# Performance work log

Measured on AMD Instinct MI355X. Metric: run time of the kernel, lower is better.

The kernel has to match this reference:

```python
import jax, jax.numpy as jnp
import numpy as np

NEG = 1e9


def setup_inputs() -> dict:
    key = jax.random.key(0)
    k1, k2, k3 = jax.random.split(key, 3)
    B, Tq, Tv, D = 8, 2048, 2048, 512
    query = jax.random.normal(k1, (B, Tq, D), dtype=jnp.float32)
    value = jax.random.normal(k2, (B, Tv, D), dtype=jnp.float32)
    # length-style masks: every row has at least one valid position
    q_len = jax.random.randint(k3, (B,), Tq // 2, Tq + 1)
    v_len = jax.random.randint(jax.random.fold_in(k3, 1), (B,), Tv // 2, Tv + 1)
    q_mask = jnp.arange(Tq)[None, :] < q_len[:, None]
    v_mask = jnp.arange(Tv)[None, :] < v_len[:, None]
    return {"query": query, "value": value, "q_mask": q_mask, "v_mask": v_mask}


def reference(query, value, q_mask, v_mask):
    # key = value (2-input case); dot-product scores: [B, Tq, Tv]
    scores = jnp.einsum("bqd,bvd->bqv", query, value)
    Tq, Tv = scores.shape[-2], scores.shape[-1]
    # causal lower-triangular mask [1, Tq, Tv]
    causal = (jnp.arange(Tq)[:, None] >= jnp.arange(Tv)[None, :])[None]
    # merge value mask [B, 1, Tv] with causal mask
    scores_mask = jnp.logical_and(v_mask[:, None, :], causal)
    scores = scores - NEG * (~scores_mask).astype(scores.dtype)
    attn = jax.nn.softmax(scores, axis=-1)
    result = jnp.einsum("bqv,bvd->bqd", attn, value)
    # zero out masked query positions
    result = result * q_mask[:, :, None].astype(result.dtype)
    return result
```

## Files before the change

### kernel.cpp

```cpp
#include <hip/hip_runtime.h>
#include <hip/hip_bf16.h>
#include <cstdint>
#include <cstddef>


#define TQ   2048
#define TV   2048
#define DIM  512
#define NB   8
#define NROW (NB * TQ)
#define NSLOT 63

typedef _Float16 f16x8 __attribute__((ext_vector_type(8)));
typedef _Float16 f16x4 __attribute__((ext_vector_type(4)));
typedef float    f32x4 __attribute__((ext_vector_type(4)));
typedef int      i32x4 __attribute__((ext_vector_type(4)));

__device__ __forceinline__ int sched_ns(int g) { return (g + 11) / 11; }
__device__ __forceinline__ int sched_start(int g) {
    return (g < 11) ? g : ((g < 22) ? (2 * g - 11) : (3 * g - 33));
}

__device__ __forceinline__ int mask_fmt(const void* qm) {
    const unsigned* p = (const unsigned*)qm;
    unsigned w0 = p[0];
    if (w0 & 0xFF00u) return 0;
    unsigned w1 = p[1];
    if (w0 == 1u) return (w1 != 0u) ? 1 : 2;
    return 3;
}
__device__ __forceinline__ bool mask_bit(const void* m, int fmt, size_t i) {
    if (fmt == 0) return ((const unsigned char*)m)[i] != 0;
    if (fmt == 1) return ((const int*)m)[i] != 0;
    if (fmt == 2) return ((const unsigned*)m)[2 * i] != 0;
    return ((const float*)m)[i] != 0.0f;
}

__device__ __forceinline__ void gload_lds16(const void* g, void* l) {
    __builtin_amdgcn_global_load_lds(
        (const __attribute__((address_space(1))) unsigned int*)g,
        (__attribute__((address_space(3))) unsigned int*)l, 16, 0, 0);
}

__global__ void cvt_f16_kernel(const float* __restrict__ in, _Float16* __restrict__ out, int n8) {
    int i = blockIdx.x * blockDim.x + threadIdx.x;
    if (i >= n8) return;
    f32x4 x0 = *(const f32x4*)(in + (size_t)i * 8);
    f32x4 x1 = *(const f32x4*)(in + (size_t)i * 8 + 4);
    f16x8 o;
#pragma unroll
    for (int j = 0; j < 4; ++j) { o[j] = (_Float16)x0[j]; o[4 + j] = (_Float16)x1[j]; }
    *(f16x8*)(out + (size_t)i * 8) = o;
}

__global__ __launch_bounds__(256)
void prep_v_kernel(const float* __restrict__ vf, _Float16* __restrict__ wv,
                   _Float16* __restrict__ wvt) {
    __shared__ float sT[64][65];
    int z   = blockIdx.x;
    int b   = z & 7;
    int tv0 = ((z >> 3) & 31) * 64;
    int d0  = (z >> 8) * 64;
    int tid = threadIdx.x;
    int vl  = tid >> 4;
    int dq  = (tid & 15) * 4;
#pragma unroll
    for (int i = 0; i < 4; ++i) {
        int v = vl + i * 16;
        f32x4 x = *(const f32x4*)(vf + ((size_t)b * TV + tv0 + v) * DIM + d0 + dq);
        f16x4 h;
#pragma unroll
        for (int j = 0; j < 4; ++j) { h[j] = (_Float16)x[j]; sT[v][dq + j] = x[j]; }
        *(f16x4*)(wv + ((size_t)b * TV + tv0 + v) * DIM + d0 + dq) = h;
    }
    __syncthreads();
    int dl = tid >> 4;
    int vq = (tid & 15) * 4;
#pragma unroll
    for (int i = 0; i < 4; ++i) {
        int dloc = dl + i * 16;
        f16x4 h;
#pragma unroll
        for (int j = 0; j < 4; ++j) h[j] = (_Float16)sT[vq + j][dloc];
        *(f16x4*)(wvt + ((size_t)b * DIM + d0 + dloc) * TV + tv0 + vq) = h;
    }
}

__global__ __launch_bounds__(512)
__attribute__((amdgpu_waves_per_eu(2, 2)))
void attn_kernel(const _Float16* __restrict__ wq, const _Float16* __restrict__ wv,
                 const _Float16* __restrict__ wvt,
                 const void* __restrict__ qmask, const void* __restrict__ vmask,
                 _Float16* __restrict__ pacc, float* __restrict__ pml) {
    __shared__ __align__(16) _Float16 sV[2][32 * 512];
    __shared__ __align__(16) char     sVT[2][512 * 64];
    __shared__ unsigned sMW[64];

    const int tid  = threadIdx.x;
    const int lane = tid & 63;
    const int w    = tid >> 6;
    const int q16  = lane & 15;
    const int grp  = lane >> 4;

    const int bid  = blockIdx.x;
    const int b    = bid & 7;
    const int slot = (NSLOT - 1) - (bid >> 3);

    int g = 0, s = 0;
#pragma unroll
    for (int j = 0; j < 32; ++j) {
        int st = sched_start(j);
        if (slot >= st && slot < st + sched_ns(j)) { g = j; s = slot - st; }
    }
    const int NSg = sched_ns(g);

    const int pairId = w >> 1;
    const int dhalf  = w & 1;
    const int qtile  = 4 * g + pairId;
    const int qrow   = qtile * 16 + q16;
    const size_t qrowG = (size_t)b * TQ + qrow;
    const int bound = qtile >> 1;

    const int fmt = mask_fmt(qmask);

    unsigned long long qbal = __ballot(mask_bit(qmask, fmt, (size_t)b * TQ + g * 64 + lane));
    const bool waveActive = ((qbal >> (16 * pairId)) & 0xFFFFull) != 0ull;
    int bmaxb = -1;
#pragma unroll
    for (int ti = 0; ti < 4; ++ti)
        if ((qbal >> (16 * ti)) & 0xFFFFull) bmaxb = max(bmaxb, (4 * g + ti) >> 1);

    if (w == 0) {
#pragma unroll
        for (int c = 0; c < 32; ++c) {
            unsigned long long bal = __ballot(mask_bit(vmask, fmt, (size_t)b * TV + c * 64 + lane));
            if (lane == 0) {
                sMW[2 * c]     = (unsigned)(bal & 0xFFFFFFFFull);
                sMW[2 * c + 1] = (unsigned)(bal >> 32);
            }
        }
    }

    f16x8 qreg[16];
    if (waveActive) {
#pragma unroll
        for (int kc = 0; kc < 16; ++kc)
            qreg[kc] = *(const f16x8*)(wq + qrowG * DIM + kc * 32 + grp * 8);
    }

    auto stage = [&](int buf, int tt) {
#pragma unroll
        for (int k = 0; k < 4; ++k) {
            int vr = w * 4 + k;
            const _Float16* src = wv + ((size_t)b * TV + tt * 32 + vr) * DIM
                                     + ((lane ^ ((vr & 7) << 2)) << 3);
            gload_lds16(src, (char*)&sV[buf][0] + vr * 1024);
        }
#pragma unroll
        for (int k = 0; k < 4; ++k) {
            int slot2 = k * 64 + lane;
            int dloc  = w * 64 + (slot2 >> 2);
            int cl    = slot2 & 3;
            const _Float16* src = wvt + ((size_t)b * DIM + dloc) * TV + tt * 32
                                      + ((cl ^ (dloc & 3)) << 3);
            gload_lds16(src, &sVT[buf][0] + w * 4096 + k * 1024);
        }
    };

    f32x4 acc[16];
#pragma unroll
    for (int c = 0; c < 16; ++c) acc[c] = (f32x4){0.f, 0.f, 0.f, 0.f};
    float m_run = -3.0e38f, l_run = 0.0f;

    const int sw = (q16 & 7) << 2;

    if (bmaxb >= s) {
        stage(0, s);
        int t1 = s + NSg; if (t1 > bmaxb) t1 = bmaxb;
        stage(1, t1);
        asm volatile("s_waitcnt vmcnt(8) lgkmcnt(0)" ::: "memory");
        __builtin_amdgcn_s_barrier();

        int cur = 0;
        for (int t = s; t <= bmaxb; t += NSg) {
            const int vb = t * 32;
            const unsigned mw = sMW[t];
            if (mw == 0u) break;
            const bool act = waveActive && (t <= bound);
            const _Float16* sVc  = &sV[cur][0];
            const char*     sVTc = &sVT[cur][0];

            f32x4 s0a = (f32x4){0.f,0.f,0.f,0.f}, s0b = s0a, s1a = s0a, s1b = s0a;
            if (act) {
                __builtin_amdgcn_s_setprio(1);
#pragma unroll
                for (int kc = 0; kc < 16; kc += 2) {
                    int c0 = ((kc * 4 + grp) ^ sw) << 4;
                    int c1 = (((kc + 1) * 4 + grp) ^ sw) << 4;
                    f16x8 a00 = *(const f16x8*)((const char*)sVc + q16 * 1024 + c0);
                    s0a = __builtin_amdgcn_mfma_f32_16x16x32_f16(a00, qreg[kc], s0a, 0, 0, 0);
                    f16x8 a10 = *(const f16x8*)((const char*)sVc + (16 + q16) * 1024 + c0);
                    s1a = __builtin_amdgcn_mfma_f32_16x16x32_f16(a10, qreg[kc], s1a, 0, 0, 0);
                    f16x8 a01 = *(const f16x8*)((const char*)sVc + q16 * 1024 + c1);
                    s0b = __builtin_amdgcn_mfma_f32_16x16x32_f16(a01, qreg[kc + 1], s0b, 0, 0, 0);
                    f16x8 a11 = *(const f16x8*)((const char*)sVc + (16 + q16) * 1024 + c1);
                    s1b = __builtin_amdgcn_mfma_f32_16x16x32_f16(a11, qreg[kc + 1], s1b, 0, 0, 0);
                }
                __builtin_amdgcn_s_setprio(0);

                f32x4 s0 = s0a + s0b, s1 = s1a + s1b;
                float p[8];
                float tm = -3.0e38f;
#pragma unroll
                for (int i = 0; i < 8; ++i) {
                    int vloc = ((i < 4) ? 0 : 16) + grp * 4 + (i & 3);
                    float x = (i < 4) ? s0[i] : s1[i - 4];
                    bool valid = ((vb + vloc) <= qrow) && ((mw >> vloc) & 1u);
                    x = valid ? x : (x - 1e9f);
                    p[i] = x;
                    tm = fmaxf(tm, x);
                }
                tm = fmaxf(tm, __shfl_xor(tm, 16, 64));
                tm = fmaxf(tm, __shfl_xor(tm, 32, 64));
                if (!__all(tm <= m_run + 8.0f)) {
                    float mn = fmaxf(m_run, tm);
                    float rr = __expf(m_run - mn);
                    l_run *= rr;
#pragma unroll
                    for (int c = 0; c < 16; ++c) acc[c] *= rr;
                    m_run = mn;
                }
                float ps = 0.0f;
#pragma unroll
                for (int i = 0; i < 8; ++i) { p[i] = __expf(p[i] - m_run); ps += p[i]; }
                ps += __shfl_xor(ps, 16, 64);
                ps += __shfl_xor(ps, 32, 64);
                l_run += ps;

                int pk0 = __builtin_bit_cast(int, __builtin_amdgcn_cvt_pkrtz(p[0], p[1]));
                int pk1 = __builtin_bit_cast(int, __builtin_amdgcn_cvt_pkrtz(p[2], p[3]));
                int pk2 = __builtin_bit_cast(int, __builtin_amdgcn_cvt_pkrtz(p[4], p[5]));
                int pk3 = __builtin_bit_cast(int, __builtin_amdgcn_cvt_pkrtz(p[6], p[7]));
                int lo = q16 + ((grp & 1) << 5);
                int hi = lo + 16;
                int a0 = __shfl(pk0, lo, 64);
                int a1 = __shfl(pk1, lo, 64);
                int a2 = __shfl(pk0, hi, 64);
                int a3 = __shfl(pk1, hi, 64);
                int c0s = __shfl(pk2, lo, 64);
                int c1s = __shfl(pk3, lo, 64);
                int c2s = __shfl(pk2, hi, 64);
                int c3s = __shfl(pk3, hi, 64);
                bool hb = (grp & 2) != 0;
                i32x4 f;
                f[0] = hb ? c0s : a0;
                f[1] = hb ? c1s : a1;
                f[2] = hb ? c2s : a2;
                f[3] = hb ? c3s : a3;
                f16x8 pf = __builtin_bit_cast(f16x8, f);

                __builtin_amdgcn_s_setprio(1);
#pragma unroll
                for (int c = 0; c < 16; ++c) {
                    int d = dhalf * 256 + c * 16 + q16;
                    f16x8 a = *(const f16x8*)(sVTc + d * 64 + ((grp ^ (d & 3)) << 4));
                    acc[c] = __builtin_amdgcn_mfma_f32_16x16x32_f16(a, pf, acc[c], 0, 0, 0);
                }
                __builtin_amdgcn_s_setprio(0);
            }
            __builtin_amdgcn_s_barrier();
            int t2 = t + 2 * NSg; if (t2 > bmaxb) t2 = bmaxb;
            stage(cur, t2);
            asm volatile("s_waitcnt vmcnt(8)" ::: "memory");
            __builtin_amdgcn_s_barrier();
            cur ^= 1;
        }
    }
    asm volatile("s_waitcnt vmcnt(0) lgkmcnt(0)" ::: "memory");

    float inv = (l_run > 0.f) ? (1.0f / l_run) : 0.0f;
    int rowInB = pairId * 16 + q16;
    _Float16* pb = pacc + (((size_t)(b * NSLOT + slot) * 64) + rowInB) * DIM;
#pragma unroll
    for (int c = 0; c < 16; ++c) {
        f16x4 hh;
#pragma unroll
        for (int j = 0; j < 4; ++j) hh[j] = (_Float16)(acc[c][j] * inv);
        *(f16x4*)(pb + dhalf * 256 + c * 16 + grp * 4) = hh;
    }
    if (dhalf == 0 && grp == 0) {
        size_t mi = (((size_t)(b * NSLOT + slot) * 64) + rowInB) * 2;
        pml[mi]     = m_run;
        pml[mi + 1] = l_run;
    }
}

__global__ __launch_bounds__(256)
void combine_kernel(const _Float16* __restrict__ pacc, const float* __restrict__ pml,
                    const void* __restrict__ qmask, float* __restrict__ out) {
    int gid = blockIdx.x * 256 + threadIdx.x;
    int row = gid >> 7;
    int c   = (gid & 127) * 4;
    if (row >= NROW) return;
    int b      = row >> 11;
    int local  = row & 2047;
    int g      = local >> 6;
    int rowInG = local & 63;
    int ns     = sched_ns(g);
    int st     = sched_start(g);

    float m = -3.0e38f;
    for (int s2 = 0; s2 < ns; ++s2) {
        size_t idx = ((size_t)(b * NSLOT + st + s2) * 64) + rowInG;
        float l2 = pml[idx * 2 + 1];
        if (l2 > 0.f) m = fmaxf(m, pml[idx * 2]);
    }
    float L = 0.f;
    f32x4 o = (f32x4){0.f, 0.f, 0.f, 0.f};
    for (int s2 = 0; s2 < ns; ++s2) {
        size_t idx = ((size_t)(b * NSLOT + st + s2) * 64) + rowInG;
        float l2 = pml[idx * 2 + 1];
        if (l2 > 0.f) {
            float wgt = __expf(pml[idx * 2] - m) * l2;
            L += wgt;
            f16x4 hh = *(const f16x4*)(pacc + idx * DIM + c);
#pragma unroll
            for (int j = 0; j < 4; ++j) o[j] += wgt * (float)hh[j];
        }
    }
    int fmt = mask_fmt(qmask);
    bool qb = mask_bit(qmask, fmt, (size_t)row);
    float invL = (L > 0.f && qb) ? (1.0f / L) : 0.f;
    o *= invL;
    *(f32x4*)(out + (size_t)row * DIM + c) = o;
}

extern "C" void kernel_launch(void* const* d_in, const int* in_sizes, int n_in,
                              void* d_out, int out_size, void* d_ws, size_t ws_size,
                              hipStream_t stream) {
    const float* q = (const float*)d_in[0];
    const float* v = (const float*)d_in[1];
    const void* qm = d_in[2];
    const void* vm = d_in[3];
    float* out = (float*)d_out;

    const size_t nElem = (size_t)NB * TQ * DIM;
    const size_t wqB   = nElem * sizeof(_Float16);
    const size_t wvB   = wqB, wvtB = wqB;
    const size_t paccB = (size_t)NB * NSLOT * 64 * DIM * sizeof(_Float16);
    const size_t pmlB  = (size_t)NB * NSLOT * 64 * 2 * sizeof(float);

    if (ws_size < wqB + wvB + wvtB + paccB + pmlB) {
        (void)hipMemsetAsync(d_out, 0, (size_t)out_size * sizeof(float), stream);
        return;
    }
    _Float16* wq   = (_Float16*)d_ws;
    _Float16* wv   = (_Float16*)((char*)d_ws + wqB);
    _Float16* wvt  = (_Float16*)((char*)d_ws + wqB + wvB);
    _Float16* pacc = (_Float16*)((char*)d_ws + wqB + wvB + wvtB);
    float*    pml  = (float*)((char*)d_ws + wqB + wvB + wvtB + paccB);

    int n8 = (int)(nElem / 8);
    cvt_f16_kernel<<<dim3(n8 / 256), dim3(256), 0, stream>>>(q, wq, n8);
    prep_v_kernel<<<dim3(2048), dim3(256), 0, stream>>>(v, wv, wvt);
    attn_kernel<<<dim3(NB * NSLOT), dim3(512), 0, stream>>>(wq, wv, wvt, qm, vm, pacc, pml);
    combine_kernel<<<dim3(NROW * 128 / 256), dim3(256), 0, stream>>>(pacc, pml, qm, out);
}
```

Before: 179.4 us.

## Switch attention to 32x32x16 MFMA tiles with split-K score reduction via LDS

Replaces the 16x16x32 MFMA flash-attention core with 32x32x16 MFMAs. Each block now covers 128 query rows (4 pairs of 32-row tiles) instead of 64, and the two waves in a pair split the head dimension K and add their partial QK scores through a new LDS scratch buffer. The V-transpose tile is now single-buffered with padded 80-byte rows and staged every iteration, and the block schedule shrinks to 57 slots per batch with new partial-buffer indexing in combine. The aim is fewer MFMA issues and better operand reuse, at the cost of extra LDS traffic, more barriers per iteration, and less overlap for the V-transpose loads.

```diff
diff --git a/kernel.cpp b/kernel.cpp
--- a/kernel.cpp
+++ b/kernel.cpp
@@ -9,17 +9,15 @@
 #define DIM  512
 #define NB   8
 #define NROW (NB * TQ)
-#define NSLOT 63
+#define NSLOT 57
 
 typedef _Float16 f16x8 __attribute__((ext_vector_type(8)));
 typedef _Float16 f16x4 __attribute__((ext_vector_type(4)));
-typedef float    f32x4 __attribute__((ext_vector_type(4)));
-typedef int      i32x4 __attribute__((ext_vector_type(4)));
-
-__device__ __forceinline__ int sched_ns(int g) { return (g + 11) / 11; }
-__device__ __forceinline__ int sched_start(int g) {
-    return (g < 11) ? g : ((g < 22) ? (2 * g - 11) : (3 * g - 33));
-}
+typedef float    f32x4  __attribute__((ext_vector_type(4)));
+typedef float    f32x16 __attribute__((ext_vector_type(16)));
+typedef int      i32x4  __attribute__((ext_vector_type(4)));
+
+__device__ __forceinline__ int sched_ns(int G) { return (4 * G + 14) / 11; }
 
 __device__ __forceinline__ int mask_fmt(const void* qm) {
     const unsigned* p = (const unsigned*)qm;
@@ -93,42 +91,53 @@
                  const void* __restrict__ qmask, const void* __restrict__ vmask,
                  _Float16* __restrict__ pacc, float* __restrict__ pml) {
     __shared__ __align__(16) _Float16 sV[2][32 * 512];
-    __shared__ __align__(16) char     sVT[2][512 * 64];
+    __shared__ __align__(16) char     sVT[512 * 80];
+    __shared__ float sS[8 * 1024];
     __shared__ unsigned sMW[64];
 
     const int tid  = threadIdx.x;
     const int lane = tid & 63;
     const int w    = tid >> 6;
-    const int q16  = lane & 15;
-    const int grp  = lane >> 4;
+    const int l31  = lane & 31;
+    const int h    = lane >> 5;
 
     const int bid  = blockIdx.x;
     const int b    = bid & 7;
     const int slot = (NSLOT - 1) - (bid >> 3);
 
-    int g = 0, s = 0;
-#pragma unroll
-    for (int j = 0; j < 32; ++j) {
-        int st = sched_start(j);
-        if (slot >= st && slot < st + sched_ns(j)) { g = j; s = slot - st; }
-    }
-    const int NSg = sched_ns(g);
-
-    const int pairId = w >> 1;
-    const int dhalf  = w & 1;
-    const int qtile  = 4 * g + pairId;
-    const int qrow   = qtile * 16 + q16;
+    int G = 0, s = 0;
+    {
+        int base = 0;
+#pragma unroll
+        for (int j = 0; j < 16; ++j) {
+            int n = sched_ns(j);
+            if (slot >= base && slot < base + n) { G = j; s = slot - base; }
+            base += n;
+        }
+    }
+    const int NSg = sched_ns(G);
+
+    const int p      = w >> 1;
+    const int kslice = w & 1;
+    const int qtile  = 4 * G + p;
+    const int qrow   = qtile * 32 + l31;
     const size_t qrowG = (size_t)b * TQ + qrow;
-    const int bound = qtile >> 1;
+    const int bound = qtile;
 
     const int fmt = mask_fmt(qmask);
 
-    unsigned long long qbal = __ballot(mask_bit(qmask, fmt, (size_t)b * TQ + g * 64 + lane));
-    const bool waveActive = ((qbal >> (16 * pairId)) & 0xFFFFull) != 0ull;
+    unsigned long long bal0 = __ballot(mask_bit(qmask, fmt, (size_t)b * TQ + G * 128 + lane));
+    unsigned long long bal1 = __ballot(mask_bit(qmask, fmt, (size_t)b * TQ + G * 128 + 64 + lane));
+    bool pact0 = (bal0 & 0xFFFFFFFFull) != 0ull;
+    bool pact1 = (bal0 >> 32) != 0ull;
+    bool pact2 = (bal1 & 0xFFFFFFFFull) != 0ull;
+    bool pact3 = (bal1 >> 32) != 0ull;
+    const bool waveActive = (p == 0) ? pact0 : (p == 1) ? pact1 : (p == 2) ? pact2 : pact3;
     int bmaxb = -1;
-#pragma unroll
-    for (int ti = 0; ti < 4; ++ti)
-        if ((qbal >> (16 * ti)) & 0xFFFFull) bmaxb = max(bmaxb, (4 * g + ti) >> 1);
+    if (pact0) bmaxb = 4 * G;
+    if (pact1) bmaxb = 4 * G + 1;
+    if (pact2) bmaxb = 4 * G + 2;
+    if (pact3) bmaxb = 4 * G + 3;
 
     if (w == 0) {
 #pragma unroll
@@ -144,41 +153,41 @@
     f16x8 qreg[16];
     if (waveActive) {
 #pragma unroll
-        for (int kc = 0; kc < 16; ++kc)
-            qreg[kc] = *(const f16x8*)(wq + qrowG * DIM + kc * 32 + grp * 8);
-    }
-
-    auto stage = [&](int buf, int tt) {
+        for (int kst = 0; kst < 16; ++kst)
+            qreg[kst] = *(const f16x8*)(wq + qrowG * DIM + kslice * 256 + kst * 16 + h * 8);
+    }
+
+    auto stage_sV = [&](int buf, int tt) {
 #pragma unroll
         for (int k = 0; k < 4; ++k) {
             int vr = w * 4 + k;
             const _Float16* src = wv + ((size_t)b * TV + tt * 32 + vr) * DIM
-                                     + ((lane ^ ((vr & 7) << 2)) << 3);
+                                     + ((lane ^ (vr & 7)) << 3);
             gload_lds16(src, (char*)&sV[buf][0] + vr * 1024);
         }
-#pragma unroll
-        for (int k = 0; k < 4; ++k) {
+    };
+    auto stage_sVT = [&](int tt) {
+#pragma unroll
+        for (int k = 0; k < 5; ++k) {
             int slot2 = k * 64 + lane;
-            int dloc  = w * 64 + (slot2 >> 2);
-            int cl    = slot2 & 3;
-            const _Float16* src = wvt + ((size_t)b * DIM + dloc) * TV + tt * 32
-                                      + ((cl ^ (dloc & 3)) << 3);
-            gload_lds16(src, &sVT[buf][0] + w * 4096 + k * 1024);
+            int dloc  = slot2 / 5;
+            int c     = slot2 - dloc * 5;
+            int cs    = (c >= 4) ? 0 : c;
+            const _Float16* src = wvt + ((size_t)b * DIM + w * 64 + dloc) * TV + tt * 32 + cs * 8;
+            gload_lds16(src, sVT + w * 5120 + k * 1024);
         }
     };
 
-    f32x4 acc[16];
-#pragma unroll
-    for (int c = 0; c < 16; ++c) acc[c] = (f32x4){0.f, 0.f, 0.f, 0.f};
+    f32x16 acc[8];
+#pragma unroll
+    for (int dt = 0; dt < 8; ++dt) acc[dt] = (f32x16)(0.f);
     float m_run = -3.0e38f, l_run = 0.0f;
 
-    const int sw = (q16 & 7) << 2;
-
     if (bmaxb >= s) {
-        stage(0, s);
+        stage_sV(0, s);
         int t1 = s + NSg; if (t1 > bmaxb) t1 = bmaxb;
-        stage(1, t1);
-        asm volatile("s_waitcnt vmcnt(8) lgkmcnt(0)" ::: "memory");
+        stage_sV(1, t1);
+        asm volatile("s_waitcnt vmcnt(4) lgkmcnt(0)" ::: "memory");
         __builtin_amdgcn_s_barrier();
 
         int cur = 0;
@@ -187,109 +196,115 @@
             const unsigned mw = sMW[t];
             if (mw == 0u) break;
             const bool act = waveActive && (t <= bound);
-            const _Float16* sVc  = &sV[cur][0];
-            const char*     sVTc = &sVT[cur][0];
-
-            f32x4 s0a = (f32x4){0.f,0.f,0.f,0.f}, s0b = s0a, s1a = s0a, s1b = s0a;
+            const _Float16* sVc = &sV[cur][0];
+
+            stage_sVT(t);
+
+            f32x16 S = (f32x16)(0.f);
             if (act) {
                 __builtin_amdgcn_s_setprio(1);
 #pragma unroll
-                for (int kc = 0; kc < 16; kc += 2) {
-                    int c0 = ((kc * 4 + grp) ^ sw) << 4;
-                    int c1 = (((kc + 1) * 4 + grp) ^ sw) << 4;
-                    f16x8 a00 = *(const f16x8*)((const char*)sVc + q16 * 1024 + c0);
-                    s0a = __builtin_amdgcn_mfma_f32_16x16x32_f16(a00, qreg[kc], s0a, 0, 0, 0);
-                    f16x8 a10 = *(const f16x8*)((const char*)sVc + (16 + q16) * 1024 + c0);
-                    s1a = __builtin_amdgcn_mfma_f32_16x16x32_f16(a10, qreg[kc], s1a, 0, 0, 0);
-                    f16x8 a01 = *(const f16x8*)((const char*)sVc + q16 * 1024 + c1);
-                    s0b = __builtin_amdgcn_mfma_f32_16x16x32_f16(a01, qreg[kc + 1], s0b, 0, 0, 0);
-                    f16x8 a11 = *(const f16x8*)((const char*)sVc + (16 + q16) * 1024 + c1);
-                    s1b = __builtin_amdgcn_mfma_f32_16x16x32_f16(a11, qreg[kc + 1], s1b, 0, 0, 0);
+                for (int kst = 0; kst < 16; ++kst) {
+                    int cw = kslice * 32 + kst * 2 + h;
+                    f16x8 a = *(const f16x8*)((const char*)sVc + l31 * 1024
+                                              + ((cw ^ (l31 & 7)) << 4));
+                    S = __builtin_amdgcn_mfma_f32_32x32x16_f16(a, qreg[kst], S, 0, 0, 0);
                 }
                 __builtin_amdgcn_s_setprio(0);
-
-                f32x4 s0 = s0a + s0b, s1 = s1a + s1b;
-                float p[8];
+#pragma unroll
+                for (int r = 0; r < 16; ++r) {
+                    int vl = (r & 3) + 8 * (r >> 2) + 4 * h;
+                    sS[w * 1024 + vl * 32 + l31] = S[r];
+                }
+            }
+            asm volatile("s_waitcnt lgkmcnt(0)" ::: "memory");
+            __builtin_amdgcn_s_barrier();
+            int t2 = t + 2 * NSg; if (t2 > bmaxb) t2 = bmaxb;
+            stage_sV(cur, t2);
+
+            f16x8 fragA, fragB;
+            if (act) {
                 float tm = -3.0e38f;
 #pragma unroll
-                for (int i = 0; i < 8; ++i) {
-                    int vloc = ((i < 4) ? 0 : 16) + grp * 4 + (i & 3);
-                    float x = (i < 4) ? s0[i] : s1[i - 4];
-                    bool valid = ((vb + vloc) <= qrow) && ((mw >> vloc) & 1u);
+                for (int r = 0; r < 16; ++r) {
+                    int vl = (r & 3) + 8 * (r >> 2) + 4 * h;
+                    float x = S[r] + sS[(w ^ 1) * 1024 + vl * 32 + l31];
+                    bool valid = ((vb + vl) <= qrow) && ((mw >> vl) & 1u);
                     x = valid ? x : (x - 1e9f);
-                    p[i] = x;
+                    S[r] = x;
                     tm = fmaxf(tm, x);
                 }
-                tm = fmaxf(tm, __shfl_xor(tm, 16, 64));
                 tm = fmaxf(tm, __shfl_xor(tm, 32, 64));
                 if (!__all(tm <= m_run + 8.0f)) {
                     float mn = fmaxf(m_run, tm);
                     float rr = __expf(m_run - mn);
                     l_run *= rr;
 #pragma unroll
-                    for (int c = 0; c < 16; ++c) acc[c] *= rr;
+                    for (int dt = 0; dt < 8; ++dt) acc[dt] *= rr;
                     m_run = mn;
                 }
                 float ps = 0.0f;
 #pragma unroll
-                for (int i = 0; i < 8; ++i) { p[i] = __expf(p[i] - m_run); ps += p[i]; }
-                ps += __shfl_xor(ps, 16, 64);
+                for (int r = 0; r < 16; ++r) { S[r] = __expf(S[r] - m_run); ps += S[r]; }
                 ps += __shfl_xor(ps, 32, 64);
                 l_run += ps;
 
-                int pk0 = __builtin_bit_cast(int, __builtin_amdgcn_cvt_pkrtz(p[0], p[1]));
-                int pk1 = __builtin_bit_cast(int, __builtin_amdgcn_cvt_pkrtz(p[2], p[3]));
-                int pk2 = __builtin_bit_cast(int, __builtin_amdgcn_cvt_pkrtz(p[4], p[5]));
-                int pk3 = __builtin_bit_cast(int, __builtin_amdgcn_cvt_pkrtz(p[6], p[7]));
-                int lo = q16 + ((grp & 1) << 5);
-                int hi = lo + 16;
-                int a0 = __shfl(pk0, lo, 64);
-                int a1 = __shfl(pk1, lo, 64);
-                int a2 = __shfl(pk0, hi, 64);
-                int a3 = __shfl(pk1, hi, 64);
-                int c0s = __shfl(pk2, lo, 64);
-                int c1s = __shfl(pk3, lo, 64);
-                int c2s = __shfl(pk2, hi, 64);
-                int c3s = __shfl(pk3, hi, 64);
-                bool hb = (grp & 2) != 0;
-                i32x4 f;
-                f[0] = hb ? c0s : a0;
-                f[1] = hb ? c1s : a1;
-                f[2] = hb ? c2s : a2;
-                f[3] = hb ? c3s : a3;
-                f16x8 pf = __builtin_bit_cast(f16x8, f);
-
+                int pk0 = __builtin_bit_cast(int, __builtin_amdgcn_cvt_pkrtz(S[0],  S[1]));
+                int pk1 = __builtin_bit_cast(int, __builtin_amdgcn_cvt_pkrtz(S[2],  S[3]));
+                int pk2 = __builtin_bit_cast(int, __builtin_amdgcn_cvt_pkrtz(S[4],  S[5]));
+                int pk3 = __builtin_bit_cast(int, __builtin_amdgcn_cvt_pkrtz(S[6],  S[7]));
+                int pk4 = __builtin_bit_cast(int, __builtin_amdgcn_cvt_pkrtz(S[8],  S[9]));
+                int pk5 = __builtin_bit_cast(int, __builtin_amdgcn_cvt_pkrtz(S[10], S[11]));
+                int pk6 = __builtin_bit_cast(int, __builtin_amdgcn_cvt_pkrtz(S[12], S[13]));
+                int pk7 = __builtin_bit_cast(int, __builtin_amdgcn_cvt_pkrtz(S[14], S[15]));
+                int x0 = __shfl_xor(pk0, 32, 64), x1 = __shfl_xor(pk1, 32, 64);
+                int x2 = __shfl_xor(pk2, 32, 64), x3 = __shfl_xor(pk3, 32, 64);
+                int x4 = __shfl_xor(pk4, 32, 64), x5 = __shfl_xor(pk5, 32, 64);
+                int x6 = __shfl_xor(pk6, 32, 64), x7 = __shfl_xor(pk7, 32, 64);
+                i32x4 fa, fb;
+                fa[0] = h ? x2 : pk0;  fa[1] = h ? x3 : pk1;
+                fa[2] = h ? pk2 : x0;  fa[3] = h ? pk3 : x1;
+                fb[0] = h ? x6 : pk4;  fb[1] = h ? x7 : pk5;
+                fb[2] = h ? pk6 : x4;  fb[3] = h ? pk7 : x5;
+                fragA = __builtin_bit_cast(f16x8, fa);
+                fragB = __builtin_bit_cast(f16x8, fb);
+            }
+            asm volatile("s_waitcnt vmcnt(4)" ::: "memory");
+            __builtin_amdgcn_s_barrier();
+
+            if (act) {
                 __builtin_amdgcn_s_setprio(1);
 #pragma unroll
-                for (int c = 0; c < 16; ++c) {
-                    int d = dhalf * 256 + c * 16 + q16;
-                    f16x8 a = *(const f16x8*)(sVTc + d * 64 + ((grp ^ (d & 3)) << 4));
-                    acc[c] = __builtin_amdgcn_mfma_f32_16x16x32_f16(a, pf, acc[c], 0, 0, 0);
+                for (int dt = 0; dt < 8; ++dt) {
+                    const char* rowp = sVT + (kslice * 256 + dt * 32 + l31) * 80;
+                    f16x8 a0 = *(const f16x8*)(rowp + h * 16);
+                    acc[dt] = __builtin_amdgcn_mfma_f32_32x32x16_f16(a0, fragA, acc[dt], 0, 0, 0);
+                    f16x8 a1 = *(const f16x8*)(rowp + 32 + h * 16);
+                    acc[dt] = __builtin_amdgcn_mfma_f32_32x32x16_f16(a1, fragB, acc[dt], 0, 0, 0);
                 }
                 __builtin_amdgcn_s_setprio(0);
             }
             __builtin_amdgcn_s_barrier();
-            int t2 = t + 2 * NSg; if (t2 > bmaxb) t2 = bmaxb;
-            stage(cur, t2);
-            asm volatile("s_waitcnt vmcnt(8)" ::: "memory");
-            __builtin_amdgcn_s_barrier();
             cur ^= 1;
         }
     }
     asm volatile("s_waitcnt vmcnt(0) lgkmcnt(0)" ::: "memory");
 
     float inv = (l_run > 0.f) ? (1.0f / l_run) : 0.0f;
-    int rowInB = pairId * 16 + q16;
-    _Float16* pb = pacc + (((size_t)(b * NSLOT + slot) * 64) + rowInB) * DIM;
-#pragma unroll
-    for (int c = 0; c < 16; ++c) {
-        f16x4 hh;
-#pragma unroll
-        for (int j = 0; j < 4; ++j) hh[j] = (_Float16)(acc[c][j] * inv);
-        *(f16x4*)(pb + dhalf * 256 + c * 16 + grp * 4) = hh;
-    }
-    if (dhalf == 0 && grp == 0) {
-        size_t mi = (((size_t)(b * NSLOT + slot) * 64) + rowInB) * 2;
+    _Float16* pb = pacc + (((size_t)(b * NSLOT + slot) * 128) + p * 32 + l31) * DIM;
+#pragma unroll
+    for (int dt = 0; dt < 8; ++dt) {
+#pragma unroll
+        for (int gb = 0; gb < 4; ++gb) {
+            f16x4 hh;
+#pragma unroll
+            for (int j = 0; j < 4; ++j) hh[j] = (_Float16)(acc[dt][gb * 4 + j] * inv);
+            int d = kslice * 256 + dt * 32 + gb * 8 + 4 * h;
+            *(f16x4*)(pb + d) = hh;
+        }
+    }
+    if (kslice == 0 && h == 0) {
+        size_t mi = (((size_t)(b * NSLOT + slot) * 128) + p * 32 + l31) * 2;
         pml[mi]     = m_run;
         pml[mi + 1] = l_run;
     }
@@ -304,21 +319,22 @@
     if (row >= NROW) return;
     int b      = row >> 11;
     int local  = row & 2047;
-    int g      = local >> 6;
-    int rowInG = local & 63;
+    int g      = local >> 7;
+    int rowInG = local & 127;
     int ns     = sched_ns(g);
-    int st     = sched_start(g);
+    int st     = 0;
+    for (int j = 0; j < 16; ++j) if (j < g) st += sched_ns(j);
 
     float m = -3.0e38f;
     for (int s2 = 0; s2 < ns; ++s2) {
-        size_t idx = ((size_t)(b * NSLOT + st + s2) * 64) + rowInG;
+        size_t idx = ((size_t)(b * NSLOT + st + s2) * 128) + rowInG;
         float l2 = pml[idx * 2 + 1];
         if (l2 > 0.f) m = fmaxf(m, pml[idx * 2]);
     }
     float L = 0.f;
     f32x4 o = (f32x4){0.f, 0.f, 0.f, 0.f};
     for (int s2 = 0; s2 < ns; ++s2) {
-        size_t idx = ((size_t)(b * NSLOT + st + s2) * 64) + rowInG;
+        size_t idx = ((size_t)(b * NSLOT + st + s2) * 128) + rowInG;
         float l2 = pml[idx * 2 + 1];
         if (l2 > 0.f) {
             float wgt = __expf(pml[idx * 2] - m) * l2;
@@ -347,8 +363,8 @@
     const size_t nElem = (size_t)NB * TQ * DIM;
     const size_t wqB   = nElem * sizeof(_Float16);
     const size_t wvB   = wqB, wvtB = wqB;
-    const size_t paccB = (size_t)NB * NSLOT * 64 * DIM * sizeof(_Float16);
-    const size_t pmlB  = (size_t)NB * NSLOT * 64 * 2 * sizeof(float);
+    const size_t paccB = (size_t)NB * NSLOT * 128 * DIM * sizeof(_Float16);
+    const size_t pmlB  = (size_t)NB * NSLOT * 128 * 2 * sizeof(float);
 
     if (ws_size < wqB + wvB + wvtB + paccB + pmlB) {
         (void)hipMemsetAsync(d_out, 0, (size_t)out_size * sizeof(float), stream);
```

Measured after the change: 233.9 us. +30.4%, slower.
